# Kernel optimization log

Hardware: AMD Instinct MI355X
Metric: run time of the kernel (lower is better)

Reference implementation:

```python
import jax, jax.numpy as jnp
import numpy as np

N_HEADS = 8
N_GROUPS = 32  # GroupNorm groups (normalization(channels) in guided-diffusion)
EPS = 1e-5


def setup_inputs() -> dict:
    key = jax.random.key(0)
    ks = jax.random.split(key, 7)
    b, c, hh, ww = 16, 512, 32, 32
    x = jax.random.normal(ks[0], (b, c, hh, ww), dtype=jnp.float32)
    norm_w = 1.0 + 0.02 * jax.random.normal(ks[1], (c,), dtype=jnp.float32)
    norm_b = 0.02 * jax.random.normal(ks[2], (c,), dtype=jnp.float32)
    # pointwise Conv1d == matmul over channels; note proj_out is zero-initialized
    # in the original, we use random weights so the op is non-trivial.
    qkv_w = jax.random.normal(ks[3], (3 * c, c), dtype=jnp.float32) / np.sqrt(c).astype(np.float32)
    qkv_b = 0.02 * jax.random.normal(ks[4], (3 * c,), dtype=jnp.float32)
    proj_w = jax.random.normal(ks[5], (c, c), dtype=jnp.float32) / np.sqrt(c).astype(np.float32)
    proj_b = 0.02 * jax.random.normal(ks[6], (c,), dtype=jnp.float32)
    return {"x": x, "norm_w": norm_w, "norm_b": norm_b,
            "qkv_w": qkv_w, "qkv_b": qkv_b, "proj_w": proj_w, "proj_b": proj_b}


def reference(x, norm_w, norm_b, qkv_w, qkv_b, proj_w, proj_b):
    b, c, hh, ww = x.shape
    t = hh * ww
    xf = x.reshape(b, c, t)

    # GroupNorm(32, c): normalize over (c//G channels, T) per group
    xg = xf.reshape(b, N_GROUPS, (c // N_GROUPS) * t)
    mu = jnp.mean(xg, axis=-1, keepdims=True)
    var = jnp.var(xg, axis=-1, keepdims=True)
    hn = ((xg - mu) * jax.lax.rsqrt(var + EPS)).reshape(b, c, t)
    hn = hn * norm_w[:, None] + norm_b[:, None]

    # pointwise conv: [b, 3c, t]
    qkv = jnp.einsum('oc,bct->bot', qkv_w, hn) + qkv_b[:, None]

    ch = c // N_HEADS
    qkv = qkv.reshape(b * N_HEADS, 3 * ch, t)
    q, k, v = jnp.split(qkv, 3, axis=1)  # each [b*H, ch, t]
    scale = np.float32(1.0 / np.sqrt(np.sqrt(ch)))
    w = jnp.einsum('bct,bcs->bts', q * scale, k * scale)  # [b*H, t, t]
    w = jax.nn.softmax(w.astype(jnp.float32), axis=-1).astype(qkv.dtype)
    a = jnp.einsum('bts,bcs->bct', w, v).reshape(b, c, t)

    h = jnp.einsum('oc,bct->bot', proj_w, a) + proj_b[:, None]
    return (xf + h).reshape(b, c, hh, ww)
```

## Files before the change

kernel.cpp:

```cpp
#include <hip/hip_runtime.h>

#define TPB 256

typedef __attribute__((ext_vector_type(8))) __bf16 bf16x8;
typedef __attribute__((ext_vector_type(4))) float f32x4;
typedef __attribute__((ext_vector_type(8))) unsigned short u16x8;
typedef __attribute__((ext_vector_type(4))) unsigned short u16x4;
typedef __attribute__((ext_vector_type(4))) unsigned int u32x4;
typedef __attribute__((ext_vector_type(2))) unsigned int u32x2;

typedef __attribute__((address_space(1))) const void gconst_void;
typedef __attribute__((address_space(3))) void lds_void;

__device__ __forceinline__ unsigned short f2bf(float f) {
  unsigned u = __builtin_bit_cast(unsigned, f);
  u += 0x7FFFu + ((u >> 16) & 1u);
  return (unsigned short)(u >> 16);
}

__device__ __forceinline__ float exp2_fast(float x) {
  float r;
  asm("v_exp_f32 %0, %1" : "=v"(r) : "v"(x));
  return r;
}

__device__ __forceinline__ float rcp_fast(float x) {
  float r;
  asm("v_rcp_f32 %0, %1" : "=v"(r) : "v"(x));
  return r;
}

__device__ __forceinline__ unsigned cvt_pk_bf16(float lo, float hi) {
  unsigned r;
  asm("v_cvt_pk_bf16_f32 %0, %1, %2" : "=v"(r) : "v"(lo), "v"(hi));
  return r;
}


__global__ __launch_bounds__(256) void k_gn_fused(const float* __restrict__ x,
                                                  const float* __restrict__ nw,
                                                  const float* __restrict__ nb,
                                                  unsigned short* __restrict__ hnT) {
  int bg = blockIdx.x;
  int b = bg >> 5, g = bg & 31;
  size_t base = (size_t)(b * 512 + g * 16) * 1024;
  const float4* p = reinterpret_cast<const float4*>(x + base);
  float s = 0.f, ss = 0.f;
#pragma unroll
  for (int i = 0; i < 16; ++i) {
    float4 v = p[threadIdx.x + i * 256];
    s += v.x + v.y + v.z + v.w;
    ss += v.x * v.x + v.y * v.y + v.z * v.z + v.w * v.w;
  }
#pragma unroll
  for (int off = 1; off < 64; off <<= 1) {
    s += __shfl_xor(s, off, 64);
    ss += __shfl_xor(ss, off, 64);
  }
  __shared__ float rbuf[4][2];
  __shared__ float stat[2];
  int wave = threadIdx.x >> 6;
  if ((threadIdx.x & 63) == 0) { rbuf[wave][0] = s; rbuf[wave][1] = ss; }
  __syncthreads();
  if (threadIdx.x == 0) {
    float S = 0.f, SS = 0.f;
    for (int i = 0; i < 4; ++i) { S += rbuf[i][0]; SS += rbuf[i][1]; }
    float m = S * (1.f / 16384.f);
    float var = SS * (1.f / 16384.f) - m * m;
    stat[0] = m;
    stat[1] = rsqrtf(var + 1e-5f);
  }
  __syncthreads();
  float mu = stat[0], rinv = stat[1];

  int tid = threadIdx.x;
#pragma unroll
  for (int q = 0; q < 2; ++q) {
    int c0 = g * 16 + q * 8;
    float a[8], bb[8];
#pragma unroll
    for (int cc = 0; cc < 8; ++cc) {
      a[cc] = rinv * nw[c0 + cc];
      bb[cc] = nb[c0 + cc] - mu * a[cc];
    }
    size_t cpart = (size_t)(c0 >> 5) * 512 + (size_t)((c0 >> 3) & 3) * 128;
#pragma unroll
    for (int it = 0; it < 4; ++it) {
      int t = it * 256 + tid;
      u16x8 o;
#pragma unroll
      for (int cc = 0; cc < 8; ++cc) {
        float v = x[base + (size_t)(q * 8 + cc) * 1024 + t];
        o[cc] = f2bf(v * a[cc] + bb[cc]);
      }
      size_t dst = (size_t)b * 524288 + (size_t)(t >> 4) * 8192 + cpart + (t & 15) * 8;
      *reinterpret_cast<u16x8*>(hnT + dst) = o;
    }
  }
}

__global__ void k_f32_to_bf16(const float* __restrict__ src, unsigned short* __restrict__ dst,
                              int n4) {
  int i = blockIdx.x * blockDim.x + threadIdx.x;
  if (i < n4) {
    float4 v = reinterpret_cast<const float4*>(src)[i];
    u16x4 o;
    o[0] = f2bf(v.x); o[1] = f2bf(v.y); o[2] = f2bf(v.z); o[3] = f2bf(v.w);
    reinterpret_cast<u16x4*>(dst)[i] = o;
  }
}

__global__ void k_pack_w(const float* __restrict__ src, unsigned short* __restrict__ dst,
                         int nchunks) {
  int i = blockIdx.x * blockDim.x + threadIdx.x;
  if (i >= nchunks) return;
  int r = i >> 6, k8 = i & 63;
  const float4* s = reinterpret_cast<const float4*>(src + (size_t)r * 512 + k8 * 8);
  float4 v0 = s[0], v1 = s[1];
  u16x8 o;
  o[0] = f2bf(v0.x); o[1] = f2bf(v0.y); o[2] = f2bf(v0.z); o[3] = f2bf(v0.w);
  o[4] = f2bf(v1.x); o[5] = f2bf(v1.y); o[6] = f2bf(v1.z); o[7] = f2bf(v1.w);
  size_t d = (size_t)(r >> 4) * 8192 + (size_t)(k8 >> 2) * 512 + (k8 & 3) * 128 + (r & 15) * 8;
  *reinterpret_cast<u16x8*>(dst + d) = o;
}

#define MFMAS(AF, BF)                                                                     \
  do {                                                                                    \
    _Pragma("unroll") for (int mi = 0; mi < 4; ++mi)                                      \
      _Pragma("unroll") for (int ni = 0; ni < 4; ++ni)                                    \
        acc[mi][ni] =                                                                     \
            __builtin_amdgcn_mfma_f32_16x16x32_bf16(AF[mi], BF[ni], acc[mi][ni], 0, 0, 0);\
  } while (0)

#define LOADT(DA, DB, kb)                                                                 \
  do {                                                                                    \
    _Pragma("unroll") for (int mi = 0; mi < 4; ++mi)                                      \
      DA[mi] = *reinterpret_cast<const bf16x8*>(pA + (size_t)mi * 8192 + (kb) * 512);     \
    _Pragma("unroll") for (int ni = 0; ni < 4; ++ni)                                      \
      DB[ni] = *reinterpret_cast<const bf16x8*>(pB + (size_t)ni * 8192 + (kb) * 512);     \
  } while (0)

__global__ __launch_bounds__(256, 2) void k_qkv_gemm(
    const unsigned short* __restrict__ hnT, const unsigned short* __restrict__ wq,
    const float* __restrict__ qkv_b, unsigned short* __restrict__ Q,
    unsigned short* __restrict__ K, unsigned short* __restrict__ V) {
  int tid = threadIdx.x;
  int lane = tid & 63, wave = tid >> 6;
  int wm = wave >> 1, wn = wave & 1;
  int g = lane >> 4, li = lane & 15;

  int wg = blockIdx.x;
  int lin = (wg & 7) * 192 + (wg >> 3);
  int bx = lin % 12;
  int tmp = lin / 12;
  int by = tmp & 7;
  int b = tmp >> 3;
  int mbase = by * 128;
  int nbase = bx * 128;

  const unsigned short* pA =
      hnT + (size_t)b * 524288 + (size_t)((mbase + wm * 64) >> 4) * 8192 + lane * 8;
  const unsigned short* pB = wq + (size_t)((nbase + wn * 64) >> 4) * 8192 + lane * 8;

  f32x4 zero = {0.f, 0.f, 0.f, 0.f};
  f32x4 acc[4][4];
#pragma unroll
  for (int mi = 0; mi < 4; ++mi)
#pragma unroll
    for (int ni = 0; ni < 4; ++ni) acc[mi][ni] = zero;

  bf16x8 a0[4], b0[4], a1[4], b1[4];
  LOADT(a0, b0, 0);
#pragma unroll
  for (int kb = 0; kb < 16; kb += 2) {
    if (kb + 1 < 16) LOADT(a1, b1, kb + 1);
    MFMAS(a0, b0);
    if (kb + 2 < 16) LOADT(a0, b0, kb + 2);
    MFMAS(a1, b1);
  }

  const float SCALE = 0.42466090143f;
#pragma unroll
  for (int ni = 0; ni < 4; ++ni) {
    int o = nbase + wn * 64 + ni * 16 + li;
    int h = o / 192;
    int j = o - h * 192;
    int bh = b * 8 + h;
    float bias = qkv_b[o];
#pragma unroll
    for (int mi = 0; mi < 4; ++mi) {
      int t0 = mbase + wm * 64 + mi * 16 + g * 4;
      f32x4 v = acc[mi][ni];
      if (j < 64) {
#pragma unroll
        for (int r = 0; r < 4; ++r)
          Q[((size_t)bh * 1024 + t0 + r) * 64 + j] = f2bf((v[r] + bias) * SCALE);
      } else if (j < 128) {
#pragma unroll
        for (int r = 0; r < 4; ++r)
          K[((size_t)bh * 1024 + t0 + r) * 64 + (j - 64)] = f2bf((v[r] + bias) * SCALE);
      } else {
        u16x4 pv;
#pragma unroll
        for (int r = 0; r < 4; ++r) pv[r] = f2bf(v[r] + bias);
        *reinterpret_cast<u16x4*>(V + ((size_t)bh * 64 + (j - 128)) * 1024 + t0) = pv;
      }
    }
  }
}

__global__ __launch_bounds__(256) void k_attn(
    const unsigned short* __restrict__ Q, const unsigned short* __restrict__ K,
    const unsigned short* __restrict__ V, unsigned short* __restrict__ aT) {
  __shared__ unsigned short Kls[2][4096];
  __shared__ unsigned short Vls[2][4096];
  int tid = threadIdx.x;
  int lane = tid & 63, w = tid >> 6;
  int g = lane >> 4, li = lane & 15;

  int wg = blockIdx.x;
  int lin = (wg & 7) * 128 + (wg >> 3);
  int qt = lin & 7;
  int bh = lin >> 3;
  int tq0 = qt * 128;
  int b = bh >> 3, h = bh & 7;

  const unsigned short* Kg = K + (size_t)bh * 1024 * 64;
  const unsigned short* Vg = V + (size_t)bh * 64 * 1024;

  bf16x8 qf[2][2];
#pragma unroll
  for (int qi = 0; qi < 2; ++qi) {
    int t = tq0 + w * 32 + qi * 16 + li;
    const unsigned short* qp = Q + ((size_t)bh * 1024 + t) * 64 + g * 8;
    qf[qi][0] = *reinterpret_cast<const bf16x8*>(qp);
    qf[qi][1] = *reinterpret_cast<const bf16x8*>(qp + 32);
  }

  int r0 = w * 16 + (lane >> 3);
  int r1 = r0 + 8;
  int h0 = (r0 ^ (r0 >> 2)) & 7;
  int h1 = (r1 ^ (r1 >> 2)) & 7;
  int c0 = ((lane & 7) ^ h0) * 8;
  int c1 = ((lane & 7) ^ h1) * 8;
  const unsigned short* kg0 = Kg + (size_t)r0 * 64 + c0;
  const unsigned short* kg1 = Kg + (size_t)r1 * 64 + c1;
  const unsigned short* vg0 = Vg + (size_t)r0 * 1024 + c0;
  const unsigned short* vg1 = Vg + (size_t)r1 * 1024 + c1;

  int srowK = ((li >> 2) << 3) | (li & 3);

  f32x4 zero = {0.f, 0.f, 0.f, 0.f};
  f32x4 oacc[2][4];
  f32x4 l_acc[2];
#pragma unroll
  for (int qi = 0; qi < 2; ++qi) {
    l_acc[qi] = zero;
#pragma unroll
    for (int nj = 0; nj < 4; ++nj) oacc[qi][nj] = zero;
  }
  u32x4 onesw = {0x3F803F80u, 0x3F803F80u, 0x3F803F80u, 0x3F803F80u};
  bf16x8 ones = __builtin_bit_cast(bf16x8, onesw);

#define ISSUE(tt, pp)                                                                    \
  do {                                                                                   \
    __builtin_amdgcn_global_load_lds((gconst_void*)(kg0 + (size_t)(tt) * 4096),          \
                                     (lds_void*)&Kls[pp][w * 1024], 16, 0, 0);           \
    __builtin_amdgcn_global_load_lds((gconst_void*)(kg1 + (size_t)(tt) * 4096),          \
                                     (lds_void*)&Kls[pp][w * 1024 + 512], 16, 0, 0);     \
    __builtin_amdgcn_global_load_lds((gconst_void*)(vg0 + (size_t)(tt) * 64),            \
                                     (lds_void*)&Vls[pp][w * 1024], 16, 0, 0);           \
    __builtin_amdgcn_global_load_lds((gconst_void*)(vg1 + (size_t)(tt) * 64),            \
                                     (lds_void*)&Vls[pp][w * 1024 + 512], 16, 0, 0);     \
  } while (0)

#define ABODY(cur)                                                                        \
  do {                                                                                    \
    const unsigned short* kbase = &Kls[cur][0];                                           \
    const unsigned short* vbase = &Vls[cur][0];                                           \
    f32x4 sacc[2][4];                                                                     \
    _Pragma("unroll") for (int ni = 0; ni < 4; ++ni) {                                    \
      int rK = ((ni >> 1) << 5) + ((ni & 1) << 2) + srowK;                                \
      int hs = ((rK ^ (rK >> 2)) & 7) << 4;                                               \
      int off0 = ((g << 4)) ^ hs;                                                         \
      int off1 = (64 + (g << 4)) ^ hs;                                                    \
      bf16x8 kf0 = *reinterpret_cast<const bf16x8*>(&kbase[rK * 64 + (off0 >> 1)]);       \
      bf16x8 kf1 = *reinterpret_cast<const bf16x8*>(&kbase[rK * 64 + (off1 >> 1)]);       \
      _Pragma("unroll") for (int qi = 0; qi < 2; ++qi) {                                  \
        f32x4 s0 = __builtin_amdgcn_mfma_f32_16x16x32_bf16(kf0, qf[qi][0], zero, 0, 0, 0);\
        sacc[qi][ni] = __builtin_amdgcn_mfma_f32_16x16x32_bf16(kf1, qf[qi][1], s0, 0, 0, 0);\
      }                                                                                   \
    }                                                                                     \
    bf16x8 pfrag[2][2];                                                                   \
    _Pragma("unroll") for (int qi = 0; qi < 2; ++qi) {                                    \
      _Pragma("unroll") for (int ni = 0; ni < 4; ++ni)                                    \
        _Pragma("unroll") for (int r = 0; r < 4; ++r)                                     \
          sacc[qi][ni][r] = exp2_fast(sacc[qi][ni][r]);                                   \
      _Pragma("unroll") for (int kk = 0; kk < 2; ++kk) {                                  \
        u32x4 pw;                                                                         \
        pw[0] = cvt_pk_bf16(sacc[qi][2 * kk][0], sacc[qi][2 * kk][1]);                    \
        pw[1] = cvt_pk_bf16(sacc[qi][2 * kk][2], sacc[qi][2 * kk][3]);                    \
        pw[2] = cvt_pk_bf16(sacc[qi][2 * kk + 1][0], sacc[qi][2 * kk + 1][1]);            \
        pw[3] = cvt_pk_bf16(sacc[qi][2 * kk + 1][2], sacc[qi][2 * kk + 1][3]);            \
        pfrag[qi][kk] = __builtin_bit_cast(bf16x8, pw);                                   \
      }                                                                                   \
      l_acc[qi] = __builtin_amdgcn_mfma_f32_16x16x32_bf16(ones, pfrag[qi][0], l_acc[qi], 0, 0, 0); \
      l_acc[qi] = __builtin_amdgcn_mfma_f32_16x16x32_bf16(ones, pfrag[qi][1], l_acc[qi], 0, 0, 0); \
    }                                                                                     \
    _Pragma("unroll") for (int nj = 0; nj < 4; ++nj) {                                    \
      int rV = nj * 16 + li;                                                              \
      int hv = ((rV ^ (rV >> 2)) & 7) << 4;                                               \
      int off0 = ((g << 4)) ^ hv;                                                         \
      int off1 = (64 + (g << 4)) ^ hv;                                                    \
      bf16x8 vf0 = *reinterpret_cast<const bf16x8*>(&vbase[rV * 64 + (off0 >> 1)]);       \
      bf16x8 vf1 = *reinterpret_cast<const bf16x8*>(&vbase[rV * 64 + (off1 >> 1)]);       \
      _Pragma("unroll") for (int qi = 0; qi < 2; ++qi) {                                  \
        oacc[qi][nj] = __builtin_amdgcn_mfma_f32_16x16x32_bf16(vf0, pfrag[qi][0], oacc[qi][nj], 0, 0, 0); \
        oacc[qi][nj] = __builtin_amdgcn_mfma_f32_16x16x32_bf16(vf1, pfrag[qi][1], oacc[qi][nj], 0, 0, 0); \
      }                                                                                   \
    }                                                                                     \
  } while (0)

  ISSUE(0, 0);
  for (int t = 0; t < 16; ++t) {
    asm volatile("s_waitcnt vmcnt(0) lgkmcnt(0)" ::: "memory");
    __builtin_amdgcn_s_barrier();
    asm volatile("" ::: "memory");
    if (t < 15) ISSUE(t + 1, (t + 1) & 1);
    ABODY(t & 1);
  }
#undef ISSUE
#undef ABODY

#pragma unroll
  for (int qi = 0; qi < 2; ++qi) {
    float inv = rcp_fast(l_acc[qi][0]);
    int t = tq0 + w * 32 + qi * 16 + li;
#pragma unroll
    for (int nj = 0; nj < 4; ++nj) {
      u32x2 ov;
      ov[0] = cvt_pk_bf16(oacc[qi][nj][0] * inv, oacc[qi][nj][1] * inv);
      ov[1] = cvt_pk_bf16(oacc[qi][nj][2] * inv, oacc[qi][nj][3] * inv);
      *reinterpret_cast<u32x2*>(aT + ((size_t)b * 1024 + t) * 512 + h * 64 + nj * 16 + g * 4) = ov;
    }
  }
}

__global__ __launch_bounds__(256) void k_proj_gemm(
    const unsigned short* __restrict__ aT, const unsigned short* __restrict__ wp,
    const float* __restrict__ proj_b, const float* __restrict__ x,
    float* __restrict__ out) {
  __shared__ unsigned short As[2][4096];
  __shared__ unsigned short Bs[2][4096];
  int tid = threadIdx.x;
  int lane = tid & 63, wave = tid >> 6;
  int wm = wave >> 1, wn = wave & 1;
  int g = lane >> 4, li = lane & 15;

  int wg = blockIdx.x;
  int lin = (wg & 7) * 64 + (wg >> 3);
  int bx = lin & 7;
  int tmp = lin >> 3;
  int by = tmp & 3;
  int b = tmp >> 2;
  int mbase = by * 128;
  int nbase = bx * 128;

  const unsigned short* Ag = wp + (size_t)mbase * 512;
  const unsigned short* Bg = aT + (size_t)b * 1024 * 512 + (size_t)nbase * 512;

  int kq = (lane & 3) ^ ((lane >> 3) & 3);
  int rst = wave * 32 + (lane >> 2);
  const char* pA0 = (const char*)Ag + (size_t)rst * 1024 + kq * 16;
  const char* pA1 = pA0 + 16 * 1024;
  const char* pB0 = (const char*)Bg + (size_t)rst * 1024 + kq * 16;
  const char* pB1 = pB0 + 16 * 1024;
  int ldsA0 = wave * 1024, ldsA1 = wave * 1024 + 512;

  int voff = 32 * li + 8 * (g ^ ((li >> 1) & 3));

  f32x4 zero = {0.f, 0.f, 0.f, 0.f};
  f32x4 acc[4][4];
#pragma unroll
  for (int mi = 0; mi < 4; ++mi)
#pragma unroll
    for (int ni = 0; ni < 4; ++ni) acc[mi][ni] = zero;

#define GISSUE(k0, buf)                                                                  \
  do {                                                                                   \
    __builtin_amdgcn_global_load_lds((gconst_void*)(pA0 + (k0) * 2),                     \
                                     (lds_void*)&As[buf][ldsA0], 16, 0, 0);              \
    __builtin_amdgcn_global_load_lds((gconst_void*)(pA1 + (k0) * 2),                     \
                                     (lds_void*)&As[buf][ldsA1], 16, 0, 0);              \
    __builtin_amdgcn_global_load_lds((gconst_void*)(pB0 + (k0) * 2),                     \
                                     (lds_void*)&Bs[buf][ldsA0], 16, 0, 0);              \
    __builtin_amdgcn_global_load_lds((gconst_void*)(pB1 + (k0) * 2),                     \
                                     (lds_void*)&Bs[buf][ldsA1], 16, 0, 0);              \
  } while (0)

  GISSUE(0, 0);
#pragma unroll
  for (int kk = 0; kk < 16; ++kk) {
    asm volatile("s_waitcnt vmcnt(0)" ::: "memory");
    __builtin_amdgcn_s_barrier();
    asm volatile("" ::: "memory");
    if (kk < 15) GISSUE((kk + 1) * 32, (kk + 1) & 1);
    const int cur = kk & 1;
    bf16x8 af[4], bfr[4];
#pragma unroll
    for (int mi = 0; mi < 4; ++mi)
      af[mi] = *reinterpret_cast<const bf16x8*>(&As[cur][wm * 2048 + mi * 512 + voff]);
#pragma unroll
    for (int ni = 0; ni < 4; ++ni)
      bfr[ni] = *reinterpret_cast<const bf16x8*>(&Bs[cur][wn * 2048 + ni * 512 + voff]);
#pragma unroll
    for (int mi = 0; mi < 4; ++mi)
#pragma unroll
      for (int ni = 0; ni < 4; ++ni)
        acc[mi][ni] = __builtin_amdgcn_mfma_f32_16x16x32_bf16(af[mi], bfr[ni], acc[mi][ni], 0, 0, 0);
  }
#undef GISSUE

#pragma unroll
  for (int mi = 0; mi < 4; ++mi) {
#pragma unroll
    for (int ni = 0; ni < 4; ++ni) {
      int t = nbase + wn * 64 + ni * 16 + li;
      f32x4 v = acc[mi][ni];
#pragma unroll
      for (int r = 0; r < 4; ++r) {
        int o = mbase + wm * 64 + mi * 16 + g * 4 + r;
        size_t idx = ((size_t)(b * 512 + o)) * 1024 + t;
        out[idx] = v[r] + proj_b[o] + x[idx];
      }
    }
  }
}

extern "C" void kernel_launch(void* const* d_in, const int* in_sizes, int n_in,
                              void* d_out, int out_size, void* d_ws, size_t ws_size,
                              hipStream_t stream) {
  (void)in_sizes; (void)n_in; (void)out_size; (void)ws_size;
  const float* x = (const float*)d_in[0];
  const float* norm_w = (const float*)d_in[1];
  const float* norm_b = (const float*)d_in[2];
  const float* qkv_w = (const float*)d_in[3];
  const float* qkv_b = (const float*)d_in[4];
  const float* proj_w = (const float*)d_in[5];
  const float* proj_b = (const float*)d_in[6];
  float* out = (float*)d_out;

  char* ws = (char*)d_ws;
  size_t off = 0;
  unsigned short* hnT = (unsigned short*)(ws + off); off += (size_t)16 * 1024 * 512 * 2;
  unsigned short* wqb = (unsigned short*)(ws + off); off += (size_t)1536 * 512 * 2;
  unsigned short* wpb = (unsigned short*)(ws + off); off += (size_t)512 * 512 * 2;
  unsigned short* Qb = (unsigned short*)(ws + off); off += (size_t)128 * 1024 * 64 * 2;
  unsigned short* Kb = (unsigned short*)(ws + off); off += (size_t)128 * 1024 * 64 * 2;
  unsigned short* Vb = (unsigned short*)(ws + off); off += (size_t)128 * 1024 * 64 * 2;

  k_gn_fused<<<512, TPB, 0, stream>>>(x, norm_w, norm_b, hnT);
  k_pack_w<<<(98304 + TPB - 1) / TPB, TPB, 0, stream>>>(qkv_w, wqb, 98304);
  k_f32_to_bf16<<<(262144 / 4 + TPB - 1) / TPB, TPB, 0, stream>>>(proj_w, wpb, 262144 / 4);
  k_qkv_gemm<<<1536, TPB, 0, stream>>>(hnT, wqb, qkv_b, Qb, Kb, Vb);
  k_attn<<<1024, TPB, 0, stream>>>(Qb, Kb, Vb, hnT );
  k_proj_gemm<<<512, TPB, 0, stream>>>(hnT, wpb, proj_b, x, out);
}
```

Measured before the change: 132.3 us.

## Pre-swizzle K/V into MFMA fragment layout and load directly from global

The QKV GEMM epilogue now writes K and V in a tiled layout that matches the per-lane MFMA fragment order. This lets the attention kernel load each fragment as one contiguous 16-byte global load per lane. The shared-memory double buffer, the barriers and the LDS swizzle reads are removed, and the loop is unrolled by two so loads can overlap compute. In exchange, every wave reloads K/V from global memory or L2 with no sharing inside the block, and the K stores in the epilogue become scattered 2-byte writes.

```diff
diff --git a/kernel.cpp b/kernel.cpp
--- a/kernel.cpp
+++ b/kernel.cpp
@@ -143,7 +143,7 @@
 __global__ __launch_bounds__(256, 2) void k_qkv_gemm(
     const unsigned short* __restrict__ hnT, const unsigned short* __restrict__ wq,
     const float* __restrict__ qkv_b, unsigned short* __restrict__ Q,
-    unsigned short* __restrict__ K, unsigned short* __restrict__ V) {
+    unsigned short* __restrict__ Kq, unsigned short* __restrict__ Vq) {
   int tid = threadIdx.x;
   int lane = tid & 63, wave = tid >> 6;
   int wm = wave >> 1, wn = wave & 1;
@@ -196,24 +196,34 @@
         for (int r = 0; r < 4; ++r)
           Q[((size_t)bh * 1024 + t0 + r) * 64 + j] = f2bf((v[r] + bias) * SCALE);
       } else if (j < 128) {
+        int ch = j - 64;
+        int kkc = ch >> 5, gk = (ch >> 3) & 3, e = ch & 7;
+        int stile = t0 >> 6, s0 = t0 & 63;
+        int nik = ((s0 >> 5) << 1) | ((s0 >> 2) & 1);
+        int lik0 = ((s0 >> 3) & 3) << 2;
+        size_t kb0 = (size_t)bh * 65536 + (size_t)stile * 4096 + nik * 1024 + kkc * 512 +
+                     gk * 128 + lik0 * 8 + e;
 #pragma unroll
         for (int r = 0; r < 4; ++r)
-          K[((size_t)bh * 1024 + t0 + r) * 64 + (j - 64)] = f2bf((v[r] + bias) * SCALE);
+          Kq[kb0 + r * 8] = f2bf((v[r] + bias) * SCALE);
       } else {
+        int ch = j - 128;
+        int nj = ch >> 4, liv = ch & 15;
+        int stile = t0 >> 6, s0 = t0 & 63;
+        int kkc = s0 >> 5, gk = (s0 >> 3) & 3, e0 = s0 & 7;
         u16x4 pv;
 #pragma unroll
         for (int r = 0; r < 4; ++r) pv[r] = f2bf(v[r] + bias);
-        *reinterpret_cast<u16x4*>(V + ((size_t)bh * 64 + (j - 128)) * 1024 + t0) = pv;
+        *reinterpret_cast<u16x4*>(Vq + (size_t)bh * 65536 + (size_t)stile * 4096 +
+                                  nj * 1024 + kkc * 512 + gk * 128 + liv * 8 + e0) = pv;
       }
     }
   }
 }
 
 __global__ __launch_bounds__(256) void k_attn(
-    const unsigned short* __restrict__ Q, const unsigned short* __restrict__ K,
-    const unsigned short* __restrict__ V, unsigned short* __restrict__ aT) {
-  __shared__ unsigned short Kls[2][4096];
-  __shared__ unsigned short Vls[2][4096];
+    const unsigned short* __restrict__ Q, const unsigned short* __restrict__ Kp,
+    const unsigned short* __restrict__ Vp, unsigned short* __restrict__ aT) {
   int tid = threadIdx.x;
   int lane = tid & 63, w = tid >> 6;
   int g = lane >> 4, li = lane & 15;
@@ -225,8 +235,8 @@
   int tq0 = qt * 128;
   int b = bh >> 3, h = bh & 7;
 
-  const unsigned short* Kg = K + (size_t)bh * 1024 * 64;
-  const unsigned short* Vg = V + (size_t)bh * 64 * 1024;
+  const unsigned short* Kb = Kp + (size_t)bh * 65536 + lane * 8;
+  const unsigned short* Vb = Vp + (size_t)bh * 65536 + lane * 8;
 
   bf16x8 qf[2][2];
 #pragma unroll
@@ -237,19 +247,6 @@
     qf[qi][1] = *reinterpret_cast<const bf16x8*>(qp + 32);
   }
 
-  int r0 = w * 16 + (lane >> 3);
-  int r1 = r0 + 8;
-  int h0 = (r0 ^ (r0 >> 2)) & 7;
-  int h1 = (r1 ^ (r1 >> 2)) & 7;
-  int c0 = ((lane & 7) ^ h0) * 8;
-  int c1 = ((lane & 7) ^ h1) * 8;
-  const unsigned short* kg0 = Kg + (size_t)r0 * 64 + c0;
-  const unsigned short* kg1 = Kg + (size_t)r1 * 64 + c1;
-  const unsigned short* vg0 = Vg + (size_t)r0 * 1024 + c0;
-  const unsigned short* vg1 = Vg + (size_t)r1 * 1024 + c1;
-
-  int srowK = ((li >> 2) << 3) | (li & 3);
-
   f32x4 zero = {0.f, 0.f, 0.f, 0.f};
   f32x4 oacc[2][4];
   f32x4 l_acc[2];
@@ -262,75 +259,55 @@
   u32x4 onesw = {0x3F803F80u, 0x3F803F80u, 0x3F803F80u, 0x3F803F80u};
   bf16x8 ones = __builtin_bit_cast(bf16x8, onesw);
 
-#define ISSUE(tt, pp)                                                                    \
-  do {                                                                                   \
-    __builtin_amdgcn_global_load_lds((gconst_void*)(kg0 + (size_t)(tt) * 4096),          \
-                                     (lds_void*)&Kls[pp][w * 1024], 16, 0, 0);           \
-    __builtin_amdgcn_global_load_lds((gconst_void*)(kg1 + (size_t)(tt) * 4096),          \
-                                     (lds_void*)&Kls[pp][w * 1024 + 512], 16, 0, 0);     \
-    __builtin_amdgcn_global_load_lds((gconst_void*)(vg0 + (size_t)(tt) * 64),            \
-                                     (lds_void*)&Vls[pp][w * 1024], 16, 0, 0);           \
-    __builtin_amdgcn_global_load_lds((gconst_void*)(vg1 + (size_t)(tt) * 64),            \
-                                     (lds_void*)&Vls[pp][w * 1024 + 512], 16, 0, 0);     \
-  } while (0)
-
-#define ABODY(cur)                                                                        \
-  do {                                                                                    \
-    const unsigned short* kbase = &Kls[cur][0];                                           \
-    const unsigned short* vbase = &Vls[cur][0];                                           \
-    f32x4 sacc[2][4];                                                                     \
-    _Pragma("unroll") for (int ni = 0; ni < 4; ++ni) {                                    \
-      int rK = ((ni >> 1) << 5) + ((ni & 1) << 2) + srowK;                                \
-      int hs = ((rK ^ (rK >> 2)) & 7) << 4;                                               \
-      int off0 = ((g << 4)) ^ hs;                                                         \
-      int off1 = (64 + (g << 4)) ^ hs;                                                    \
-      bf16x8 kf0 = *reinterpret_cast<const bf16x8*>(&kbase[rK * 64 + (off0 >> 1)]);       \
-      bf16x8 kf1 = *reinterpret_cast<const bf16x8*>(&kbase[rK * 64 + (off1 >> 1)]);       \
-      _Pragma("unroll") for (int qi = 0; qi < 2; ++qi) {                                  \
-        f32x4 s0 = __builtin_amdgcn_mfma_f32_16x16x32_bf16(kf0, qf[qi][0], zero, 0, 0, 0);\
-        sacc[qi][ni] = __builtin_amdgcn_mfma_f32_16x16x32_bf16(kf1, qf[qi][1], s0, 0, 0, 0);\
-      }                                                                                   \
-    }                                                                                     \
-    bf16x8 pfrag[2][2];                                                                   \
-    _Pragma("unroll") for (int qi = 0; qi < 2; ++qi) {                                    \
-      _Pragma("unroll") for (int ni = 0; ni < 4; ++ni)                                    \
-        _Pragma("unroll") for (int r = 0; r < 4; ++r)                                     \
-          sacc[qi][ni][r] = exp2_fast(sacc[qi][ni][r]);                                   \
-      _Pragma("unroll") for (int kk = 0; kk < 2; ++kk) {                                  \
-        u32x4 pw;                                                                         \
-        pw[0] = cvt_pk_bf16(sacc[qi][2 * kk][0], sacc[qi][2 * kk][1]);                    \
-        pw[1] = cvt_pk_bf16(sacc[qi][2 * kk][2], sacc[qi][2 * kk][3]);                    \
-        pw[2] = cvt_pk_bf16(sacc[qi][2 * kk + 1][0], sacc[qi][2 * kk + 1][1]);            \
-        pw[3] = cvt_pk_bf16(sacc[qi][2 * kk + 1][2], sacc[qi][2 * kk + 1][3]);            \
-        pfrag[qi][kk] = __builtin_bit_cast(bf16x8, pw);                                   \
-      }                                                                                   \
-      l_acc[qi] = __builtin_amdgcn_mfma_f32_16x16x32_bf16(ones, pfrag[qi][0], l_acc[qi], 0, 0, 0); \
-      l_acc[qi] = __builtin_amdgcn_mfma_f32_16x16x32_bf16(ones, pfrag[qi][1], l_acc[qi], 0, 0, 0); \
-    }                                                                                     \
-    _Pragma("unroll") for (int nj = 0; nj < 4; ++nj) {                                    \
-      int rV = nj * 16 + li;                                                              \
-      int hv = ((rV ^ (rV >> 2)) & 7) << 4;                                               \
-      int off0 = ((g << 4)) ^ hv;                                                         \
-      int off1 = (64 + (g << 4)) ^ hv;                                                    \
-      bf16x8 vf0 = *reinterpret_cast<const bf16x8*>(&vbase[rV * 64 + (off0 >> 1)]);       \
-      bf16x8 vf1 = *reinterpret_cast<const bf16x8*>(&vbase[rV * 64 + (off1 >> 1)]);       \
-      _Pragma("unroll") for (int qi = 0; qi < 2; ++qi) {                                  \
-        oacc[qi][nj] = __builtin_amdgcn_mfma_f32_16x16x32_bf16(vf0, pfrag[qi][0], oacc[qi][nj], 0, 0, 0); \
-        oacc[qi][nj] = __builtin_amdgcn_mfma_f32_16x16x32_bf16(vf1, pfrag[qi][1], oacc[qi][nj], 0, 0, 0); \
-      }                                                                                   \
-    }                                                                                     \
-  } while (0)
-
-  ISSUE(0, 0);
+#pragma unroll 2
   for (int t = 0; t < 16; ++t) {
-    asm volatile("s_waitcnt vmcnt(0) lgkmcnt(0)" ::: "memory");
-    __builtin_amdgcn_s_barrier();
-    asm volatile("" ::: "memory");
-    if (t < 15) ISSUE(t + 1, (t + 1) & 1);
-    ABODY(t & 1);
-  }
-#undef ISSUE
-#undef ABODY
+    const unsigned short* kt = Kb + (size_t)t * 4096;
+    const unsigned short* vt = Vb + (size_t)t * 4096;
+    bf16x8 kf[8], vf[8];
+#pragma unroll
+    for (int i = 0; i < 8; ++i) kf[i] = *reinterpret_cast<const bf16x8*>(kt + i * 512);
+#pragma unroll
+    for (int i = 0; i < 8; ++i) vf[i] = *reinterpret_cast<const bf16x8*>(vt + i * 512);
+
+    f32x4 sacc[2][4];
+#pragma unroll
+    for (int ni = 0; ni < 4; ++ni) {
+#pragma unroll
+      for (int qi = 0; qi < 2; ++qi) {
+        f32x4 s0 = __builtin_amdgcn_mfma_f32_16x16x32_bf16(kf[ni * 2 + 0], qf[qi][0], zero, 0, 0, 0);
+        sacc[qi][ni] = __builtin_amdgcn_mfma_f32_16x16x32_bf16(kf[ni * 2 + 1], qf[qi][1], s0, 0, 0, 0);
+      }
+    }
+
+    bf16x8 pfrag[2][2];
+#pragma unroll
+    for (int qi = 0; qi < 2; ++qi) {
+#pragma unroll
+      for (int ni = 0; ni < 4; ++ni)
+#pragma unroll
+        for (int r = 0; r < 4; ++r) sacc[qi][ni][r] = exp2_fast(sacc[qi][ni][r]);
+#pragma unroll
+      for (int kk = 0; kk < 2; ++kk) {
+        u32x4 pw;
+        pw[0] = cvt_pk_bf16(sacc[qi][2 * kk][0], sacc[qi][2 * kk][1]);
+        pw[1] = cvt_pk_bf16(sacc[qi][2 * kk][2], sacc[qi][2 * kk][3]);
+        pw[2] = cvt_pk_bf16(sacc[qi][2 * kk + 1][0], sacc[qi][2 * kk + 1][1]);
+        pw[3] = cvt_pk_bf16(sacc[qi][2 * kk + 1][2], sacc[qi][2 * kk + 1][3]);
+        pfrag[qi][kk] = __builtin_bit_cast(bf16x8, pw);
+      }
+      l_acc[qi] = __builtin_amdgcn_mfma_f32_16x16x32_bf16(ones, pfrag[qi][0], l_acc[qi], 0, 0, 0);
+      l_acc[qi] = __builtin_amdgcn_mfma_f32_16x16x32_bf16(ones, pfrag[qi][1], l_acc[qi], 0, 0, 0);
+    }
+
+#pragma unroll
+    for (int nj = 0; nj < 4; ++nj) {
+#pragma unroll
+      for (int qi = 0; qi < 2; ++qi) {
+        oacc[qi][nj] = __builtin_amdgcn_mfma_f32_16x16x32_bf16(vf[nj * 2 + 0], pfrag[qi][0], oacc[qi][nj], 0, 0, 0);
+        oacc[qi][nj] = __builtin_amdgcn_mfma_f32_16x16x32_bf16(vf[nj * 2 + 1], pfrag[qi][1], oacc[qi][nj], 0, 0, 0);
+      }
+    }
+  }
 
 #pragma unroll
   for (int qi = 0; qi < 2; ++qi) {
```

Measured after the change: 177.2 us. 33.9% more time.
